# Kernel tuning notes

Measured on AMD Instinct MI355X. Metric: run time of the kernel, lower is better.

The kernel has to match this reference:

```python
import jax, jax.numpy as jnp
import numpy as np

V = 2562
DEG = 8
NNZ = V * DEG
B, FIN, FOUT, K = 1, 8, 16, 5
X = Y = Z = 8


def setup_inputs() -> dict:
    key = jax.random.key(0)
    k1, k2, k3, k4, k5 = jax.random.split(key, 5)
    inputs = jax.random.normal(k1, (B, FIN, V, X, Y, Z), dtype=jnp.float32)
    # COO sparse Laplacian: each vertex has DEG entries (valid row indices)
    lap_rows = jnp.repeat(jnp.arange(V, dtype=jnp.int32), DEG)
    lap_cols = jax.random.randint(k2, (NNZ,), 0, V, dtype=jnp.int32)
    lap_vals = jax.random.normal(k3, (NNZ,), dtype=jnp.float32) * 0.1
    std = np.sqrt(2.0 / (FIN * K)).astype(np.float32)
    weight = jax.random.normal(k4, (K, FIN, FOUT), dtype=jnp.float32) * std
    bias = jnp.full((FOUT,), 0.01, dtype=jnp.float32)
    return {"inputs": inputs, "lap_rows": lap_rows, "lap_cols": lap_cols,
            "lap_vals": lap_vals, "weight": weight, "bias": bias}


def _spmv(vals, rows, cols, x):
    # sparse [V,V] @ dense [V,D] via gather + segment_sum
    return jax.ops.segment_sum(vals[:, None] * x[cols], rows, num_segments=V)


def reference(inputs, lap_rows, lap_cols, lap_vals, weight, bias):
    # x0: [V, Fin*B*X*Y*Z]
    x0 = jnp.transpose(inputs, (2, 1, 0, 3, 4, 5)).reshape(V, FIN * B * X * Y * Z)
    xs = [x0]
    if K > 1:
        x1 = _spmv(lap_vals, lap_rows, lap_cols, x0)
        xs.append(x1)
        for _ in range(2, K):
            x2 = 2.0 * _spmv(lap_vals, lap_rows, lap_cols, x1) - x0
            xs.append(x2)
            x0, x1 = x1, x2
    cheb = jnp.stack(xs, 0).reshape(K, V, FIN, B, X, Y, Z)
    # matmul over (K, Fin): out [B, Fout, V, X, Y, Z]
    out = jnp.einsum('kvfbxyz,kfo->bovxyz', cheb, weight)
    out = out + bias[None, :, None, None, None, None]
    return out
```

## Files before the change

kernel.cpp:

```cpp
#include <hip/hip_runtime.h>
#include <hip/hip_bf16.h>

constexpr int V_    = 2562;
constexpr int DEG_  = 8;
constexpr int FIN_  = 8;
constexpr int FOUT_ = 16;
constexpr int S_    = 512;
constexpr int VS_   = V_ * S_;
constexpr int VP_   = 2564;
constexpr int LSTR  = 12;
constexpr long INT_PLANE = (long)S_ * VP_;
constexpr int TPB   = 1024;
constexpr int NV    = 3;

__device__ __forceinline__ float4 ld4(const float* p) {
    return *reinterpret_cast<const float4*>(p);
}
__device__ __forceinline__ void st4(float* p, float4 v) {
    *reinterpret_cast<float4*>(p) = v;
}
__device__ __forceinline__ ushort f2bf_bits(float x) {
    __hip_bfloat16 h = __float2bfloat16(x);
    return *reinterpret_cast<ushort*>(&h);
}
__device__ __forceinline__ float bf2f_bits(ushort u) {
    return __uint_as_float((unsigned)u << 16);
}

__global__ __launch_bounds__(256)
void transpose_k(const float* __restrict__ src, float* __restrict__ dst,
                 int M, int N, long srcZ, long dstZ, int dstStride)
{
    __shared__ float tile[64][65];
    const long zs = (long)blockIdx.z * srcZ;
    const long zd = (long)blockIdx.z * dstZ;
    const int n0 = blockIdx.x * 64;
    const int m0 = blockIdx.y * 64;
    const int t  = threadIdx.x;
    const int q  = t & 15;
    const int r  = t >> 4;

#pragma unroll
    for (int i = 0; i < 4; ++i) {
        const int m = m0 + r + i * 16;
        const int n = n0 + q * 4;
        if (m < M && n < N) {
            const float4 x = ld4(src + zs + (long)m * N + n);
            tile[r + i * 16][q * 4 + 0] = x.x;
            tile[r + i * 16][q * 4 + 1] = x.y;
            tile[r + i * 16][q * 4 + 2] = x.z;
            tile[r + i * 16][q * 4 + 3] = x.w;
        }
    }
    __syncthreads();
#pragma unroll
    for (int i = 0; i < 4; ++i) {
        const int n = n0 + r + i * 16;
        const int m = m0 + q * 4;
        if (n < N && (m + 4) <= dstStride) {
            const float4 x = make_float4(tile[q * 4 + 0][r + i * 16],
                                         tile[q * 4 + 1][r + i * 16],
                                         tile[q * 4 + 2][r + i * 16],
                                         tile[q * 4 + 3][r + i * 16]);
            st4(dst + zd + (long)n * dstStride + m, x);
        }
    }
}

__global__ __launch_bounds__(TPB)
void cheb_rec(const float* __restrict__ inT,
              const int*   __restrict__ cols,
              const float* __restrict__ vals,
              ushort* __restrict__ cheb)
{
    extern __shared__ float cur[];
    const int s = blockIdx.x;
    const int t = threadIdx.x;

    {
        const int f = t & 7;
        const int cb = t >> 3;
        const float* plane = inT + (long)f * INT_PLANE + (long)s * VP_;
        for (int c = cb; c < VP_ / 4; c += TPB / 8) {
            const float4 x = ld4(plane + c * 4);
            cur[(c * 4 + 0) * LSTR + f] = x.x;
            cur[(c * 4 + 1) * LSTR + f] = x.y;
            cur[(c * 4 + 2) * LSTR + f] = x.z;
            cur[(c * 4 + 3) * LSTR + f] = x.w;
        }
    }
    __syncthreads();

    float xp[NV][8];
#pragma unroll
    for (int j = 0; j < NV; ++j) {
        const int v = (t + j * TPB < V_) ? (t + j * TPB) : 0;
        const float4 lo = ld4(&cur[v * LSTR]);
        const float4 hi = ld4(&cur[v * LSTR + 4]);
        xp[j][0] = lo.x; xp[j][1] = lo.y; xp[j][2] = lo.z; xp[j][3] = lo.w;
        xp[j][4] = hi.x; xp[j][5] = hi.y; xp[j][6] = hi.z; xp[j][7] = hi.w;
    }

#pragma unroll 1
    for (int k = 1; k < 5; ++k) {
        float xk[NV][8];
#pragma unroll
        for (int j = 0; j < NV; ++j) {
            const bool valid = (t + j * TPB) < V_;
            const int v = valid ? (t + j * TPB) : 0;
            int off = v * 8;
            asm volatile("" : "+v"(off));
            const int4   ca = *reinterpret_cast<const int4*>(cols + off);
            const int4   cb = *reinterpret_cast<const int4*>(cols + off + 4);
            const float4 wa = ld4(vals + off);
            const float4 wb = ld4(vals + off + 4);
            const int   cc[8] = {ca.x, ca.y, ca.z, ca.w, cb.x, cb.y, cb.z, cb.w};
            const float ww[8] = {wa.x, wa.y, wa.z, wa.w, wb.x, wb.y, wb.z, wb.w};

            float a[8];
#pragma unroll
            for (int e = 0; e < 8; ++e) a[e] = 0.f;
#pragma unroll
            for (int n = 0; n < 8; ++n) {
                const float* p = &cur[cc[n] * LSTR];
                const float4 lo = ld4(p);
                const float4 hi = ld4(p + 4);
                const float w = ww[n];
                a[0] = fmaf(w, lo.x, a[0]); a[1] = fmaf(w, lo.y, a[1]);
                a[2] = fmaf(w, lo.z, a[2]); a[3] = fmaf(w, lo.w, a[3]);
                a[4] = fmaf(w, hi.x, a[4]); a[5] = fmaf(w, hi.y, a[5]);
                a[6] = fmaf(w, hi.z, a[6]); a[7] = fmaf(w, hi.w, a[7]);
            }
#pragma unroll
            for (int e = 0; e < 8; ++e)
                xk[j][e] = (k == 1) ? a[e] : fmaf(2.f, a[e], -xp[j][e]);

            if (valid) {
                union { ushort u[8]; int4 q; } pk;
#pragma unroll
                for (int f = 0; f < 8; ++f)
                    pk.u[f] = f2bf_bits(xk[j][f]);
                *reinterpret_cast<int4*>(
                    cheb + (((long)(k - 1) * S_ + s) * V_ + v) * 8) = pk.q;
            }

            if (k < 4) {
                const float4 lo = ld4(&cur[v * LSTR]);
                const float4 hi = ld4(&cur[v * LSTR + 4]);
                xp[j][0] = lo.x; xp[j][1] = lo.y; xp[j][2] = lo.z; xp[j][3] = lo.w;
                xp[j][4] = hi.x; xp[j][5] = hi.y; xp[j][6] = hi.z; xp[j][7] = hi.w;
            }
        }
        if (k < 4) {
            __syncthreads();
#pragma unroll
            for (int j = 0; j < NV; ++j) {
                const int vr = t + j * TPB;
                if (vr < V_) {
                    st4(&cur[vr * LSTR],
                        make_float4(xk[j][0], xk[j][1], xk[j][2], xk[j][3]));
                    st4(&cur[vr * LSTR + 4],
                        make_float4(xk[j][4], xk[j][5], xk[j][6], xk[j][7]));
                }
            }
            __syncthreads();
        }
    }
}

__global__ __launch_bounds__(TPB)
void proj(const float* __restrict__ in,
          const ushort* __restrict__ cheb,
          const float* __restrict__ W,
          const float* __restrict__ bias,
          float* __restrict__ out)
{
    __shared__ float smem[8 * 64 * 17];
    const int v0 = blockIdx.x * 64;
    const int s0 = blockIdx.y * 16;
    const int t  = threadIdx.x;

#pragma unroll
    for (int p = 0; p < 2; ++p) {
        const int idx = t + p * TPB;
        const int sq  = idx & 3;
        const int v   = (idx >> 2) & 63;
        const int f   = idx >> 8;
        const int vg  = (v0 + v < V_) ? (v0 + v) : (V_ - 1);
        const float4 x = ld4(in + (long)f * VS_ + (long)vg * S_ + s0 + sq * 4);
        float* d = &smem[f * 1088 + v * 17 + sq * 4];
        d[0] = x.x; d[1] = x.y; d[2] = x.z; d[3] = x.w;
    }
    __syncthreads();

    const int tv = t & 63;
    const int ts = t >> 6;
    const int vg = (v0 + tv < V_) ? (v0 + tv) : (V_ - 1);

    float acc[16];
#pragma unroll
    for (int o = 0; o < 16; ++o) acc[o] = bias[o];

#pragma unroll
    for (int f = 0; f < FIN_; ++f) {
        const float xv = smem[f * 1088 + tv * 17 + ts];
#pragma unroll
        for (int o = 0; o < 16; ++o)
            acc[o] = fmaf(W[f * 16 + o], xv, acc[o]);
    }
#pragma unroll
    for (int k = 1; k < 5; ++k) {
        union { int4 q; ushort u[8]; } pk;
        pk.q = *reinterpret_cast<const int4*>(
            cheb + (((long)(k - 1) * S_ + (s0 + ts)) * V_ + vg) * 8);
        float xv[8];
#pragma unroll
        for (int f = 0; f < 8; ++f)
            xv[f] = bf2f_bits(pk.u[f]);
#pragma unroll
        for (int f = 0; f < 8; ++f) {
#pragma unroll
            for (int o = 0; o < 16; ++o)
                acc[o] = fmaf(W[(k * 8 + f) * 16 + o], xv[f], acc[o]);
        }
    }

#pragma unroll
    for (int h = 0; h < 2; ++h) {
        __syncthreads();
#pragma unroll
        for (int ol = 0; ol < 8; ++ol)
            smem[ol * 1088 + tv * 17 + ts] = acc[h * 8 + ol];
        __syncthreads();
#pragma unroll
        for (int p = 0; p < 2; ++p) {
            const int idx = t + p * TPB;
            const int sq  = idx & 3;
            const int v   = (idx >> 2) & 63;
            const int ol  = idx >> 8;
            if (v0 + v < V_) {
                const float* r = &smem[ol * 1088 + v * 17 + sq * 4];
                st4(out + (long)(h * 8 + ol) * VS_ + (long)(v0 + v) * S_ + s0 + sq * 4,
                    make_float4(r[0], r[1], r[2], r[3]));
            }
        }
    }
}

extern "C" void kernel_launch(void* const* d_in, const int* in_sizes, int n_in,
                              void* d_out, int out_size, void* d_ws, size_t ws_size,
                              hipStream_t stream) {
    const float* in   = (const float*)d_in[0];
    const int*   cols = (const int*)d_in[2];
    const float* vals = (const float*)d_in[3];
    const float* W    = (const float*)d_in[4];
    const float* bias = (const float*)d_in[5];
    float* out = (float*)d_out;

    float* inT = out;
    ushort* cheb = (ushort*)d_ws;

    (void)hipFuncSetAttribute((const void*)cheb_rec,
                              hipFuncAttributeMaxDynamicSharedMemorySize,
                              VP_ * LSTR * (int)sizeof(float));

    transpose_k<<<dim3(8, 41, 8), 256, 0, stream>>>(
        in, inT, V_, S_, (long)VS_, INT_PLANE, VP_);

    cheb_rec<<<dim3(S_), TPB, VP_ * LSTR * (int)sizeof(float), stream>>>(
        inT, cols, vals, cheb);

    proj<<<dim3(41, 32), TPB, 0, stream>>>(in, cheb, W, bias, out);
}
```

Measured before the change: 210.4 us.

## Pack two spatial slices as half2 in Chebyshev recurrence and store cheb as fp16

The Chebyshev recurrence kernel now processes two spatial positions per block, packing them into __half2 in LDS and using packed hfma2 arithmetic, which halves the block count and the per-element gather and FMA instructions. The intermediate cheb buffer changes from bf16 to fp16, and the projection kernel decodes it accordingly. This trades numerical accuracy for throughput: the recurrence now accumulates in fp16 rather than fp32, the Laplacian weights are rounded to half, and fp16 has less range than bf16. Larger values from repeated recurrence steps could lose precision.

```diff
diff --git a/kernel.cpp b/kernel.cpp
--- a/kernel.cpp
+++ b/kernel.cpp
@@ -1,5 +1,6 @@
 #include <hip/hip_runtime.h>
 #include <hip/hip_bf16.h>
+#include <hip/hip_fp16.h>
 
 constexpr int V_    = 2562;
 constexpr int DEG_  = 8;
@@ -19,12 +20,14 @@
 __device__ __forceinline__ void st4(float* p, float4 v) {
     *reinterpret_cast<float4*>(p) = v;
 }
-__device__ __forceinline__ ushort f2bf_bits(float x) {
-    __hip_bfloat16 h = __float2bfloat16(x);
-    return *reinterpret_cast<ushort*>(&h);
-}
-__device__ __forceinline__ float bf2f_bits(ushort u) {
-    return __uint_as_float((unsigned)u << 16);
+__device__ __forceinline__ unsigned h2bits(__half2 h) {
+    union { __half2 h; unsigned u; } c; c.h = h; return c.u;
+}
+__device__ __forceinline__ __half2 bits2h(unsigned u) {
+    union { unsigned u; __half2 h; } c; c.u = u; return c.h;
+}
+__device__ __forceinline__ unsigned packh2(float e, float o) {
+    return h2bits(__halves2half2(__float2half(e), __float2half(o)));
 }
 
 __global__ __launch_bounds__(256)
@@ -73,37 +76,43 @@
               const float* __restrict__ vals,
               ushort* __restrict__ cheb)
 {
-    extern __shared__ float cur[];
-    const int s = blockIdx.x;
-    const int t = threadIdx.x;
+    extern __shared__ unsigned cur[];
+    const int s2 = blockIdx.x * 2;
+    const int t  = threadIdx.x;
 
     {
-        const int f = t & 7;
+        const int f  = t & 7;
         const int cb = t >> 3;
-        const float* plane = inT + (long)f * INT_PLANE + (long)s * VP_;
+        const float* pe = inT + (long)f * INT_PLANE + (long)s2 * VP_;
+        const float* po = pe + VP_;
         for (int c = cb; c < VP_ / 4; c += TPB / 8) {
-            const float4 x = ld4(plane + c * 4);
-            cur[(c * 4 + 0) * LSTR + f] = x.x;
-            cur[(c * 4 + 1) * LSTR + f] = x.y;
-            cur[(c * 4 + 2) * LSTR + f] = x.z;
-            cur[(c * 4 + 3) * LSTR + f] = x.w;
+            const float4 xe = ld4(pe + c * 4);
+            const float4 xo = ld4(po + c * 4);
+            cur[(c * 4 + 0) * LSTR + f] = packh2(xe.x, xo.x);
+            cur[(c * 4 + 1) * LSTR + f] = packh2(xe.y, xo.y);
+            cur[(c * 4 + 2) * LSTR + f] = packh2(xe.z, xo.z);
+            cur[(c * 4 + 3) * LSTR + f] = packh2(xe.w, xo.w);
         }
     }
     __syncthreads();
 
-    float xp[NV][8];
+    const __half2 two2 = __half2half2(__float2half(2.0f));
+
+    __half2 xp[NV][8];
 #pragma unroll
     for (int j = 0; j < NV; ++j) {
         const int v = (t + j * TPB < V_) ? (t + j * TPB) : 0;
-        const float4 lo = ld4(&cur[v * LSTR]);
-        const float4 hi = ld4(&cur[v * LSTR + 4]);
-        xp[j][0] = lo.x; xp[j][1] = lo.y; xp[j][2] = lo.z; xp[j][3] = lo.w;
-        xp[j][4] = hi.x; xp[j][5] = hi.y; xp[j][6] = hi.z; xp[j][7] = hi.w;
+        const uint4 lo = *reinterpret_cast<const uint4*>(&cur[v * LSTR]);
+        const uint4 hi = *reinterpret_cast<const uint4*>(&cur[v * LSTR + 4]);
+        xp[j][0] = bits2h(lo.x); xp[j][1] = bits2h(lo.y);
+        xp[j][2] = bits2h(lo.z); xp[j][3] = bits2h(lo.w);
+        xp[j][4] = bits2h(hi.x); xp[j][5] = bits2h(hi.y);
+        xp[j][6] = bits2h(hi.z); xp[j][7] = bits2h(hi.w);
     }
 
 #pragma unroll 1
     for (int k = 1; k < 5; ++k) {
-        float xk[NV][8];
+        __half2 xk[NV][8];
 #pragma unroll
         for (int j = 0; j < NV; ++j) {
             const bool valid = (t + j * TPB) < V_;
@@ -117,38 +126,52 @@
             const int   cc[8] = {ca.x, ca.y, ca.z, ca.w, cb.x, cb.y, cb.z, cb.w};
             const float ww[8] = {wa.x, wa.y, wa.z, wa.w, wb.x, wb.y, wb.z, wb.w};
 
-            float a[8];
-#pragma unroll
-            for (int e = 0; e < 8; ++e) a[e] = 0.f;
+            __half2 a[8];
+#pragma unroll
+            for (int e = 0; e < 8; ++e) a[e] = bits2h(0u);
 #pragma unroll
             for (int n = 0; n < 8; ++n) {
-                const float* p = &cur[cc[n] * LSTR];
-                const float4 lo = ld4(p);
-                const float4 hi = ld4(p + 4);
-                const float w = ww[n];
-                a[0] = fmaf(w, lo.x, a[0]); a[1] = fmaf(w, lo.y, a[1]);
-                a[2] = fmaf(w, lo.z, a[2]); a[3] = fmaf(w, lo.w, a[3]);
-                a[4] = fmaf(w, hi.x, a[4]); a[5] = fmaf(w, hi.y, a[5]);
-                a[6] = fmaf(w, hi.z, a[6]); a[7] = fmaf(w, hi.w, a[7]);
+                const unsigned* p = &cur[cc[n] * LSTR];
+                const uint4 lo = *reinterpret_cast<const uint4*>(p);
+                const uint4 hi = *reinterpret_cast<const uint4*>(p + 4);
+                const __half2 w2 = __half2half2(__float2half(ww[n]));
+                a[0] = __hfma2(w2, bits2h(lo.x), a[0]);
+                a[1] = __hfma2(w2, bits2h(lo.y), a[1]);
+                a[2] = __hfma2(w2, bits2h(lo.z), a[2]);
+                a[3] = __hfma2(w2, bits2h(lo.w), a[3]);
+                a[4] = __hfma2(w2, bits2h(hi.x), a[4]);
+                a[5] = __hfma2(w2, bits2h(hi.y), a[5]);
+                a[6] = __hfma2(w2, bits2h(hi.z), a[6]);
+                a[7] = __hfma2(w2, bits2h(hi.w), a[7]);
             }
 #pragma unroll
             for (int e = 0; e < 8; ++e)
-                xk[j][e] = (k == 1) ? a[e] : fmaf(2.f, a[e], -xp[j][e]);
+                xk[j][e] = (k == 1) ? a[e]
+                                    : __hfma2(two2, a[e], __hneg2(xp[j][e]));
 
             if (valid) {
-                union { ushort u[8]; int4 q; } pk;
-#pragma unroll
-                for (int f = 0; f < 8; ++f)
-                    pk.u[f] = f2bf_bits(xk[j][f]);
-                *reinterpret_cast<int4*>(
-                    cheb + (((long)(k - 1) * S_ + s) * V_ + v) * 8) = pk.q;
+                unsigned ue[4], uo[4];
+#pragma unroll
+                for (int i = 0; i < 4; ++i) {
+                    const unsigned b0 = h2bits(xk[j][2 * i]);
+                    const unsigned b1 = h2bits(xk[j][2 * i + 1]);
+                    ue[i] = __builtin_amdgcn_perm(b1, b0, 0x05040100u);
+                    uo[i] = __builtin_amdgcn_perm(b1, b0, 0x07060302u);
+                }
+                const long base = (((long)(k - 1) * S_ + s2) * V_ + v) * 8;
+                *reinterpret_cast<uint4*>(cheb + base) =
+                    make_uint4(ue[0], ue[1], ue[2], ue[3]);
+                *reinterpret_cast<uint4*>(cheb + base + (long)V_ * 8) =
+                    make_uint4(uo[0], uo[1], uo[2], uo[3]);
             }
 
             if (k < 4) {
-                const float4 lo = ld4(&cur[v * LSTR]);
-                const float4 hi = ld4(&cur[v * LSTR + 4]);
-                xp[j][0] = lo.x; xp[j][1] = lo.y; xp[j][2] = lo.z; xp[j][3] = lo.w;
-                xp[j][4] = hi.x; xp[j][5] = hi.y; xp[j][6] = hi.z; xp[j][7] = hi.w;
+                const uint4 lo = *reinterpret_cast<const uint4*>(&cur[v * LSTR]);
+                const uint4 hi = *reinterpret_cast<const uint4*>(&cur[v * LSTR + 4]);
+                xp[j][0] = bits2h(lo.x); xp[j][1] = bits2h(lo.y);
+                xp[j][2] = bits2h(lo.z); xp[j][3] = bits2h(lo.w);
+                xp[j][4] = bits2h(hi.x); xp[j][5] = bits2h(hi.y);
+                xp[j][6] = bits2h(hi.z); xp[j][7] = bits2h(hi.w);
             }
         }
         if (k < 4) {
@@ -157,10 +180,12 @@
             for (int j = 0; j < NV; ++j) {
                 const int vr = t + j * TPB;
                 if (vr < V_) {
-                    st4(&cur[vr * LSTR],
-                        make_float4(xk[j][0], xk[j][1], xk[j][2], xk[j][3]));
-                    st4(&cur[vr * LSTR + 4],
-                        make_float4(xk[j][4], xk[j][5], xk[j][6], xk[j][7]));
+                    *reinterpret_cast<uint4*>(&cur[vr * LSTR]) =
+                        make_uint4(h2bits(xk[j][0]), h2bits(xk[j][1]),
+                                   h2bits(xk[j][2]), h2bits(xk[j][3]));
+                    *reinterpret_cast<uint4*>(&cur[vr * LSTR + 4]) =
+                        make_uint4(h2bits(xk[j][4]), h2bits(xk[j][5]),
+                                   h2bits(xk[j][6]), h2bits(xk[j][7]));
                 }
             }
             __syncthreads();
@@ -210,13 +235,13 @@
     }
 #pragma unroll
     for (int k = 1; k < 5; ++k) {
-        union { int4 q; ushort u[8]; } pk;
+        union { int4 q; __half u[8]; } pk;
         pk.q = *reinterpret_cast<const int4*>(
             cheb + (((long)(k - 1) * S_ + (s0 + ts)) * V_ + vg) * 8);
         float xv[8];
 #pragma unroll
         for (int f = 0; f < 8; ++f)
-            xv[f] = bf2f_bits(pk.u[f]);
+            xv[f] = __half2float(pk.u[f]);
 #pragma unroll
         for (int f = 0; f < 8; ++f) {
 #pragma unroll
@@ -262,12 +287,12 @@
 
     (void)hipFuncSetAttribute((const void*)cheb_rec,
                               hipFuncAttributeMaxDynamicSharedMemorySize,
-                              VP_ * LSTR * (int)sizeof(float));
+                              VP_ * LSTR * (int)sizeof(unsigned));
 
     transpose_k<<<dim3(8, 41, 8), 256, 0, stream>>>(
         in, inT, V_, S_, (long)VS_, INT_PLANE, VP_);
 
-    cheb_rec<<<dim3(S_), TPB, VP_ * LSTR * (int)sizeof(float), stream>>>(
+    cheb_rec<<<dim3(S_ / 2), TPB, VP_ * LSTR * (int)sizeof(unsigned), stream>>>(
         inT, cols, vals, cheb);
 
     proj<<<dim3(41, 32), TPB, 0, stream>>>(in, cheb, W, bias, out);
```

After: 196.8 us. 1.07x faster.
